# Optimization experiments

Hardware: AMD Instinct MI355X
Metric: run time of the kernel (lower is better)

Reference implementation:

```python
import jax, jax.numpy as jnp
import numpy as np

N = 100000
E = 1600000
D = 128


def setup_inputs() -> dict:
    key = jax.random.key(0)
    ks = jax.random.split(key, 16)
    inp = {
        "x": jax.random.normal(ks[0], (N, D), dtype=jnp.float32),
        "src": jax.random.randint(ks[1], (E,), 0, N, dtype=jnp.int32),
        "dst": jax.random.randint(ks[2], (E,), 0, N, dtype=jnp.int32),
    }
    scale = 1.0 / np.sqrt(D)
    for i in range(4):
        inp[f"ws{i}"] = jax.random.normal(ks[3 + 3 * i], (D, D), dtype=jnp.float32) * scale
        inp[f"wn{i}"] = jax.random.normal(ks[4 + 3 * i], (D, D), dtype=jnp.float32) * scale
        inp[f"b{i}"] = jnp.zeros((D,), dtype=jnp.float32)
    return inp


def _sage_layer(h, src, dst, w_self, w_neigh, b):
    # gather source-node features along edges, mean-reduce by destination
    msg = jnp.take(h, src, axis=0)                                   # [E, D]
    agg = jax.ops.segment_sum(msg, dst, num_segments=N)              # [N, D]
    deg = jax.ops.segment_sum(jnp.ones_like(dst, dtype=h.dtype), dst, num_segments=N)
    mean = agg / jnp.maximum(deg, 1.0)[:, None]                      # zero-degree -> 0
    return h @ w_self + mean @ w_neigh + b


def reference(x, src, dst, ws0, wn0, b0, ws1, wn1, b1, ws2, wn2, b2, ws3, wn3, b3):
    h = jax.nn.relu(_sage_layer(x, src, dst, ws0, wn0, b0))
    h = jax.nn.relu(_sage_layer(h, src, dst, ws1, wn1, b1))
    h = jax.nn.relu(_sage_layer(h, src, dst, ws2, wn2, b2))
    h = _sage_layer(h, src, dst, ws3, wn3, b3)
    return h
```

## Files before the change

kernel.cpp:

```cpp
#include <hip/hip_runtime.h>

#define N_NODES 100000
#define N_EDGES 1600000
#define DIM 128

typedef __attribute__((ext_vector_type(8))) _Float16 f16x8;
typedef __attribute__((ext_vector_type(4))) float f32x4;

__device__ __forceinline__ void stage16(const _Float16* g, _Float16* l) {
  __builtin_amdgcn_global_load_lds(
      (const __attribute__((address_space(1))) void*)g,
      (__attribute__((address_space(3))) void*)l, 16, 0, 0);
}


__global__ void k_count(const int* __restrict__ dst, int* __restrict__ cnt) {
  int i = blockIdx.x * blockDim.x + threadIdx.x;
  if (i < N_EDGES) atomicAdd(&cnt[dst[i]], 1);
}

__global__ void k_scan_blk(const int* __restrict__ cnt, int* __restrict__ offs,
                           int* __restrict__ partials) {
  int tid = threadIdx.x;
  int gid = blockIdx.x * 1024 + tid;
  int v = (gid < N_NODES) ? cnt[gid] : 0;
  int lane = tid & 63, w = tid >> 6;
  int s = v;
#pragma unroll
  for (int d = 1; d < 64; d <<= 1) {
    int t = __shfl_up(s, d);
    if (lane >= d) s += t;
  }
  __shared__ int wsum[16];
  if (lane == 63) wsum[w] = s;
  __syncthreads();
  if (tid < 16) {
    int t2 = wsum[tid];
#pragma unroll
    for (int d = 1; d < 16; d <<= 1) {
      int u = __shfl_up(t2, d);
      if (tid >= d) t2 += u;
    }
    wsum[tid] = t2;
  }
  __syncthreads();
  if (w > 0) s += wsum[w - 1];
  if (gid < N_NODES) offs[gid + 1] = s;
  if (tid == 1023) partials[blockIdx.x] = s;
}

__global__ void k_scan_part(int* __restrict__ partials, int nb) {
  __shared__ int tmp[128];
  int tid = threadIdx.x;
  tmp[tid] = (tid < nb) ? partials[tid] : 0;
  __syncthreads();
  for (int d = 1; d < 128; d <<= 1) {
    int t = (tid >= d) ? tmp[tid - d] : 0;
    __syncthreads();
    tmp[tid] += t;
    __syncthreads();
  }
  if (tid < nb) partials[tid] = (tid > 0) ? tmp[tid - 1] : 0;
}

__global__ void k_scan_add(int* __restrict__ offs, const int* __restrict__ partials) {
  int i = blockIdx.x * blockDim.x + threadIdx.x;
  if (i == 0) offs[0] = 0;
  if (i < N_NODES) offs[i + 1] += partials[i >> 10];
}

__global__ void k_prep(const int* __restrict__ offs, const int* __restrict__ cnt,
                       int* __restrict__ cursor, float* __restrict__ deg_inv) {
  int i = blockIdx.x * blockDim.x + threadIdx.x;
  if (i < N_NODES) {
    cursor[i] = offs[i];
    deg_inv[i] = 1.0f / (float)max(cnt[i], 1);
  }
}

#define FILL_BPP 224
__global__ void k_fill8(const int* __restrict__ src, const int* __restrict__ dst,
                        int* __restrict__ cursor, int* __restrict__ esrc) {
  const int part = blockIdx.x & 7;
  const int bp = blockIdx.x >> 3;
  const int lo = part * (N_NODES / 8);
  const int hi = lo + (N_NODES / 8);
  for (int i = bp * 256 + threadIdx.x; i < N_EDGES; i += FILL_BPP * 256) {
    int d = dst[i];
    if (d >= lo && d < hi) {
      int p = atomicAdd(&cursor[d], 1);
      esrc[p] = src[i];
    }
  }
}


#define WP_MAT (4 * 8 * 64 * 8)
#define WP_LAYER (2 * WP_MAT)

#define NZ_BLOCKS ((N_NODES + 255) / 256)
#define NX_BLOCKS ((N_NODES * DIM / 4 + 255) / 256)
#define NW_BLOCKS 64

__global__ void k_preproc(int* __restrict__ cnt, const float* __restrict__ x,
                          _Float16* __restrict__ x1, _Float16* __restrict__ x2,
                          const float* __restrict__ ws0, const float* __restrict__ wn0,
                          const float* __restrict__ ws1, const float* __restrict__ wn1,
                          const float* __restrict__ ws2, const float* __restrict__ wn2,
                          const float* __restrict__ ws3, const float* __restrict__ wn3,
                          _Float16* __restrict__ wp) {
  const int bid = blockIdx.x;
  if (bid < NZ_BLOCKS) {
    int i = bid * 256 + threadIdx.x;
    if (i < N_NODES) cnt[i] = 0;
  } else if (bid < NZ_BLOCKS + NX_BLOCKS) {
    int i = (bid - NZ_BLOCKS) * 256 + threadIdx.x;
    if (i < (N_NODES * DIM) / 4) {
      float4 v = reinterpret_cast<const float4*>(x)[i];
      union { _Float16 h[4]; uint2 u; } a, b;
      float vv[4] = {v.x, v.y, v.z, v.w};
#pragma unroll
      for (int j = 0; j < 4; ++j) {
        _Float16 h1 = (_Float16)vv[j];
        a.h[j] = h1;
        b.h[j] = (_Float16)(vv[j] - (float)h1);
      }
      reinterpret_cast<uint2*>(x1)[i] = a.u;
      reinterpret_cast<uint2*>(x2)[i] = b.u;
    }
  } else {
    int tid = (bid - NZ_BLOCKS - NX_BLOCKS) * 256 + threadIdx.x;
    int l = tid & 63;
    int f = (tid >> 6) & 7;
    int t = (tid >> 9) & 3;
    int m = (tid >> 11) & 1;
    int layer = tid >> 12;
    const float* srcs[8] = {ws0, wn0, ws1, wn1, ws2, wn2, ws3, wn3};
    const float* src = srcs[layer * 2 + m];
    _Float16* dstp =
        wp + (size_t)layer * WP_LAYER + ((((m * 4 + t) * 8 + f) * 64 + l) * 8);
    int k0 = t * 32 + (l >> 4) * 8;
    int col = f * 16 + (l & 15);
#pragma unroll
    for (int j = 0; j < 8; ++j) dstp[j] = (_Float16)src[(k0 + j) * DIM + col];
  }
}


__device__ __forceinline__ float f16lo(unsigned w) {
  union { unsigned u; _Float16 h[2]; } c;
  c.u = w;
  return (float)c.h[0];
}
__device__ __forceinline__ float f16hi(unsigned w) {
  union { unsigned u; _Float16 h[2]; } c;
  c.u = w;
  return (float)c.h[1];
}

__global__ void k_agg_f16(const _Float16* __restrict__ h1, const int* __restrict__ offs,
                          const int* __restrict__ esrc, const float* __restrict__ deg_inv,
                          _Float16* __restrict__ m1) {
  int wid = (blockIdx.x * blockDim.x + threadIdx.x) >> 6;
  int lane = threadIdx.x & 63;
  if (wid >= N_NODES) return;
  const unsigned* H = reinterpret_cast<const unsigned*>(h1);
  int beg = offs[wid], end = offs[wid + 1];
  float xs[8] = {0.f, 0.f, 0.f, 0.f, 0.f, 0.f, 0.f, 0.f};
  float ys[8] = {0.f, 0.f, 0.f, 0.f, 0.f, 0.f, 0.f, 0.f};
  int e = beg;
  for (; e + 7 < end; e += 8) {
    int s[8];
#pragma unroll
    for (int j = 0; j < 8; ++j) s[j] = esrc[e + j];
    unsigned w[8];
#pragma unroll
    for (int j = 0; j < 8; ++j) w[j] = H[(size_t)s[j] * 64 + lane];
#pragma unroll
    for (int j = 0; j < 8; ++j) {
      xs[j] += f16lo(w[j]);
      ys[j] += f16hi(w[j]);
    }
  }
  for (; e + 1 < end; e += 2) {
    unsigned w0 = H[(size_t)esrc[e] * 64 + lane];
    unsigned w1 = H[(size_t)esrc[e + 1] * 64 + lane];
    xs[0] += f16lo(w0); ys[0] += f16hi(w0);
    xs[1] += f16lo(w1); ys[1] += f16hi(w1);
  }
  if (e < end) {
    unsigned w0 = H[(size_t)esrc[e] * 64 + lane];
    xs[2] += f16lo(w0); ys[2] += f16hi(w0);
  }
  float di = deg_inv[wid];
  float rx = ((xs[0] + xs[1]) + (xs[2] + xs[3])) + ((xs[4] + xs[5]) + (xs[6] + xs[7]));
  float ry = ((ys[0] + ys[1]) + (ys[2] + ys[3])) + ((ys[4] + ys[5]) + (ys[6] + ys[7]));
  rx *= di;
  ry *= di;
  union { unsigned u; _Float16 h[2]; } o;
  o.h[0] = (_Float16)rx;
  o.h[1] = (_Float16)ry;
  reinterpret_cast<unsigned*>(m1)[(size_t)wid * 64 + lane] = o.u;
}


template <int RELU, int LAST>
__global__ __launch_bounds__(256, 3) void k_gemm_f16(
    const _Float16* __restrict__ hp1, const _Float16* __restrict__ hp2,
    const _Float16* __restrict__ mp1, const _Float16* __restrict__ wp,
    const float* __restrict__ bias, float* __restrict__ outf,
    _Float16* __restrict__ o1, _Float16* __restrict__ o2) {
  __shared__ _Float16 sA[3][64 * 128];

  const int tid = threadIdx.x;
  const int lane = tid & 63;
  const int wv = tid >> 6;
  const int wr = wv >> 1;
  const int wc = wv & 1;
  const int row0 = blockIdx.x * 64;
  const int lr = lane & 15;
  const int lg = lane >> 4;

  const _Float16* planes[3] = {hp1, hp2, mp1};

#pragma unroll
  for (int p = 0; p < 3; ++p)
#pragma unroll
    for (int i = 0; i < 4; ++i) {
      int s = i * 256 + tid;
      int row = s >> 4;
      int chunk = (s & 15) ^ (row & 7);
      const _Float16* g = planes[p] + (size_t)(row0 + row) * DIM + chunk * 8;
      _Float16* l = &sA[p][(size_t)(i * 256 + (tid & ~63)) * 8];
      stage16(g, l);
    }
  __syncthreads();

  f32x4 acc[2][4];
#pragma unroll
  for (int i = 0; i < 2; ++i)
#pragma unroll
    for (int j = 0; j < 4; ++j) acc[i][j] = (f32x4){0.f, 0.f, 0.f, 0.f};

  const _Float16* WS1 = wp;
  const _Float16* WN1 = wp + WP_MAT;

#pragma unroll
  for (int t = 0; t < 4; ++t) {
    f16x8 a1[2], a2[2], am[2];
#pragma unroll
    for (int ri = 0; ri < 2; ++ri) {
      int row_l = wr * 32 + ri * 16 + lr;
      int boff = (row_l << 8) + ((t * 64 + lg * 16) ^ ((row_l & 7) << 4));
      a1[ri] = *reinterpret_cast<const f16x8*>(
          reinterpret_cast<const char*>(&sA[0][0]) + boff);
      a2[ri] = *reinterpret_cast<const f16x8*>(
          reinterpret_cast<const char*>(&sA[1][0]) + boff);
      am[ri] = *reinterpret_cast<const f16x8*>(
          reinterpret_cast<const char*>(&sA[2][0]) + boff);
    }
#pragma unroll
    for (int fc = 0; fc < 4; ++fc) {
      int f = wc * 4 + fc;
      size_t boff = (size_t)((t * 8 + f) * 64 + lane) * 8;
      f16x8 bs1 = *reinterpret_cast<const f16x8*>(WS1 + boff);
      f16x8 bn1 = *reinterpret_cast<const f16x8*>(WN1 + boff);
#pragma unroll
      for (int ri = 0; ri < 2; ++ri) {
        acc[ri][fc] =
            __builtin_amdgcn_mfma_f32_16x16x32_f16(a1[ri], bs1, acc[ri][fc], 0, 0, 0);
        acc[ri][fc] =
            __builtin_amdgcn_mfma_f32_16x16x32_f16(a2[ri], bs1, acc[ri][fc], 0, 0, 0);
        acc[ri][fc] =
            __builtin_amdgcn_mfma_f32_16x16x32_f16(am[ri], bn1, acc[ri][fc], 0, 0, 0);
      }
    }
  }

  float bv[4];
#pragma unroll
  for (int fc = 0; fc < 4; ++fc) bv[fc] = bias[wc * 64 + fc * 16 + lr];
#pragma unroll
  for (int ri = 0; ri < 2; ++ri)
#pragma unroll
    for (int fc = 0; fc < 4; ++fc)
#pragma unroll
      for (int r = 0; r < 4; ++r) {
        int row = row0 + wr * 32 + ri * 16 + lg * 4 + r;
        if (row < N_NODES) {
          float v = acc[ri][fc][r] + bv[fc];
          if (RELU) v = fmaxf(v, 0.f);
          size_t idx = (size_t)row * DIM + wc * 64 + fc * 16 + lr;
          if (LAST) {
            outf[idx] = v;
          } else {
            _Float16 hi = (_Float16)v;
            o1[idx] = hi;
            o2[idx] = (_Float16)(v - (float)hi);
          }
        }
      }
}


extern "C" void kernel_launch(void* const* d_in, const int* in_sizes, int n_in,
                              void* d_out, int out_size, void* d_ws, size_t ws_size,
                              hipStream_t stream) {
  const float* x = (const float*)d_in[0];
  const int* src = (const int*)d_in[1];
  const int* dst = (const int*)d_in[2];
  const float* Ws[4];
  const float* Wn[4];
  const float* Bi[4];
  for (int i = 0; i < 4; ++i) {
    Ws[i] = (const float*)d_in[3 + 3 * i];
    Wn[i] = (const float*)d_in[4 + 3 * i];
    Bi[i] = (const float*)d_in[5 + 3 * i];
  }
  float* out = (float*)d_out;

  char* p = (char*)d_ws;
  auto take = [&](size_t bytes) {
    void* r = (void*)p;
    p += (bytes + 255) & ~(size_t)255;
    return r;
  };
  int* cnt = (int*)take((size_t)N_NODES * 4);
  int* offs = (int*)take((size_t)(N_NODES + 1) * 4);
  int* cursor = (int*)take((size_t)N_NODES * 4);
  int* partials = (int*)take(128 * 4);
  float* deg_inv = (float*)take((size_t)N_NODES * 4);
  int* esrc = (int*)take((size_t)N_EDGES * 4);
  _Float16* hA1 = (_Float16*)take((size_t)N_NODES * DIM * 2);
  _Float16* hA2 = (_Float16*)take((size_t)N_NODES * DIM * 2);
  _Float16* hB1 = (_Float16*)take((size_t)N_NODES * DIM * 2);
  _Float16* hB2 = (_Float16*)take((size_t)N_NODES * DIM * 2);
  _Float16* m1 = (_Float16*)take((size_t)N_NODES * DIM * 2);
  _Float16* wpk = (_Float16*)take((size_t)4 * WP_LAYER * 2);
  (void)take((size_t)64 * 1024);

  const int NB = (N_NODES + 1023) / 1024;

  k_preproc<<<NZ_BLOCKS + NX_BLOCKS + NW_BLOCKS, 256, 0, stream>>>(
      cnt, x, hA1, hA2, Ws[0], Wn[0], Ws[1], Wn[1], Ws[2], Wn[2], Ws[3], Wn[3], wpk);

  k_count<<<(N_EDGES + 255) / 256, 256, 0, stream>>>(dst, cnt);
  k_scan_blk<<<NB, 1024, 0, stream>>>(cnt, offs, partials);
  k_scan_part<<<1, 128, 0, stream>>>(partials, NB);
  k_scan_add<<<(N_NODES + 255) / 256, 256, 0, stream>>>(offs, partials);
  k_prep<<<(N_NODES + 255) / 256, 256, 0, stream>>>(offs, cnt, cursor, deg_inv);
  k_fill8<<<8 * FILL_BPP, 256, 0, stream>>>(src, dst, cursor, esrc);

  const int AGG_BLOCKS = (N_NODES + 3) / 4;
  const int GEMM_BLOCKS = (N_NODES + 63) / 64;

  _Float16 *h1 = hA1, *h2 = hA2, *n1 = hB1, *n2 = hB2;
  for (int l = 0; l < 4; ++l) {
    k_agg_f16<<<AGG_BLOCKS, 256, 0, stream>>>(h1, offs, esrc, deg_inv, m1);
    const _Float16* wl = wpk + (size_t)l * WP_LAYER;
    if (l < 3) {
      k_gemm_f16<1, 0><<<GEMM_BLOCKS, 256, 0, stream>>>(h1, h2, m1, wl, Bi[l], nullptr,
                                                        n1, n2);
      _Float16* t1 = h1; h1 = n1; n1 = t1;
      _Float16* t2 = h2; h2 = n2; n2 = t2;
    } else {
      k_gemm_f16<0, 1><<<GEMM_BLOCKS, 256, 0, stream>>>(h1, h2, m1, wl, Bi[l], out,
                                                        nullptr, nullptr);
    }
  }
}
```

Before: 552.4 us.

## Slice hi-half features into 16-column planes for cache-local aggregation

Stores the fp16 high part of node features in a column-sliced layout with 8 planes of 16 features per node. The aggregation kernel now runs one block group per slice, so each wave gathers 32-byte pieces from a 3.2 MB plane that can stay cache-resident, and combines partial sums across 8 edge groups with shuffles. The GEMM loader and epilogue are updated to read and write the sliced layout. In exchange it launches 8x more aggregation blocks, re-reads the edge index list once per slice, and the GEMM's hi-part stores become more scattered.

```diff
diff --git a/kernel.cpp b/kernel.cpp
--- a/kernel.cpp
+++ b/kernel.cpp
@@ -103,7 +103,7 @@
 #define NW_BLOCKS 64
 
 __global__ void k_preproc(int* __restrict__ cnt, const float* __restrict__ x,
-                          _Float16* __restrict__ x1, _Float16* __restrict__ x2,
+                          _Float16* __restrict__ x1t, _Float16* __restrict__ x2,
                           const float* __restrict__ ws0, const float* __restrict__ wn0,
                           const float* __restrict__ ws1, const float* __restrict__ wn1,
                           const float* __restrict__ ws2, const float* __restrict__ wn2,
@@ -125,7 +125,11 @@
         a.h[j] = h1;
         b.h[j] = (_Float16)(vv[j] - (float)h1);
       }
-      reinterpret_cast<uint2*>(x1)[i] = a.u;
+      int flat = i * 4;
+      int n = flat >> 7;
+      int d = flat & 127;
+      _Float16* dsta = x1t + ((size_t)(d >> 4) * N_NODES + n) * 16 + (d & 15);
+      *reinterpret_cast<uint2*>(dsta) = a.u;
       reinterpret_cast<uint2*>(x2)[i] = b.u;
     }
   } else {
@@ -158,58 +162,59 @@
   return (float)c.h[1];
 }
 
-__global__ void k_agg_f16(const _Float16* __restrict__ h1, const int* __restrict__ offs,
-                          const int* __restrict__ esrc, const float* __restrict__ deg_inv,
-                          _Float16* __restrict__ m1) {
-  int wid = (blockIdx.x * blockDim.x + threadIdx.x) >> 6;
-  int lane = threadIdx.x & 63;
-  if (wid >= N_NODES) return;
-  const unsigned* H = reinterpret_cast<const unsigned*>(h1);
-  int beg = offs[wid], end = offs[wid + 1];
-  float xs[8] = {0.f, 0.f, 0.f, 0.f, 0.f, 0.f, 0.f, 0.f};
-  float ys[8] = {0.f, 0.f, 0.f, 0.f, 0.f, 0.f, 0.f, 0.f};
-  int e = beg;
-  for (; e + 7 < end; e += 8) {
-    int s[8];
-#pragma unroll
-    for (int j = 0; j < 8; ++j) s[j] = esrc[e + j];
-    unsigned w[8];
-#pragma unroll
-    for (int j = 0; j < 8; ++j) w[j] = H[(size_t)s[j] * 64 + lane];
-#pragma unroll
-    for (int j = 0; j < 8; ++j) {
-      xs[j] += f16lo(w[j]);
-      ys[j] += f16hi(w[j]);
-    }
-  }
-  for (; e + 1 < end; e += 2) {
-    unsigned w0 = H[(size_t)esrc[e] * 64 + lane];
-    unsigned w1 = H[(size_t)esrc[e + 1] * 64 + lane];
-    xs[0] += f16lo(w0); ys[0] += f16hi(w0);
-    xs[1] += f16lo(w1); ys[1] += f16hi(w1);
-  }
-  if (e < end) {
-    unsigned w0 = H[(size_t)esrc[e] * 64 + lane];
-    xs[2] += f16lo(w0); ys[2] += f16hi(w0);
-  }
-  float di = deg_inv[wid];
-  float rx = ((xs[0] + xs[1]) + (xs[2] + xs[3])) + ((xs[4] + xs[5]) + (xs[6] + xs[7]));
-  float ry = ((ys[0] + ys[1]) + (ys[2] + ys[3])) + ((ys[4] + ys[5]) + (ys[6] + ys[7]));
-  rx *= di;
-  ry *= di;
-  union { unsigned u; _Float16 h[2]; } o;
-  o.h[0] = (_Float16)rx;
-  o.h[1] = (_Float16)ry;
-  reinterpret_cast<unsigned*>(m1)[(size_t)wid * 64 + lane] = o.u;
+__global__ __launch_bounds__(256) void k_agg_t(
+    const _Float16* __restrict__ h1t, const int* __restrict__ offs,
+    const int* __restrict__ esrc, const float* __restrict__ deg_inv,
+    _Float16* __restrict__ m1) {
+  const int slice = blockIdx.x & 7;
+  const int node = (blockIdx.x >> 3) * 4 + (threadIdx.x >> 6);
+  if (node >= N_NODES) return;
+  const int lane = threadIdx.x & 63;
+  const int g = lane >> 3;
+  const int d = lane & 7;
+  const unsigned* T =
+      reinterpret_cast<const unsigned*>(h1t) + (size_t)slice * N_NODES * 8;
+  int beg = offs[node], end = offs[node + 1];
+  float ax = 0.f, ay = 0.f, bx = 0.f, by = 0.f;
+  for (int e = beg; e < end; e += 16) {
+    int e0 = e + g;
+    int e1 = e + 8 + g;
+    if (e0 < end) {
+      int s0 = __builtin_nontemporal_load(esrc + e0);
+      unsigned w0 = T[(size_t)s0 * 8 + d];
+      ax += f16lo(w0);
+      ay += f16hi(w0);
+    }
+    if (e1 < end) {
+      int s1 = __builtin_nontemporal_load(esrc + e1);
+      unsigned w1 = T[(size_t)s1 * 8 + d];
+      bx += f16lo(w1);
+      by += f16hi(w1);
+    }
+  }
+  ax += bx;
+  ay += by;
+#pragma unroll
+  for (int m = 8; m < 64; m <<= 1) {
+    ax += __shfl_xor(ax, m);
+    ay += __shfl_xor(ay, m);
+  }
+  if (lane < 8) {
+    float di = deg_inv[node];
+    union { unsigned u; _Float16 h[2]; } o;
+    o.h[0] = (_Float16)(ax * di);
+    o.h[1] = (_Float16)(ay * di);
+    reinterpret_cast<unsigned*>(m1)[(size_t)node * 64 + slice * 8 + d] = o.u;
+  }
 }
 
 
 template <int RELU, int LAST>
 __global__ __launch_bounds__(256, 3) void k_gemm_f16(
-    const _Float16* __restrict__ hp1, const _Float16* __restrict__ hp2,
+    const _Float16* __restrict__ h1t, const _Float16* __restrict__ hp2,
     const _Float16* __restrict__ mp1, const _Float16* __restrict__ wp,
     const float* __restrict__ bias, float* __restrict__ outf,
-    _Float16* __restrict__ o1, _Float16* __restrict__ o2) {
+    _Float16* __restrict__ o1t, _Float16* __restrict__ o2) {
   __shared__ _Float16 sA[3][64 * 128];
 
   const int tid = threadIdx.x;
@@ -221,18 +226,25 @@
   const int lr = lane & 15;
   const int lg = lane >> 4;
 
-  const _Float16* planes[3] = {hp1, hp2, mp1};
-
-#pragma unroll
-  for (int p = 0; p < 3; ++p)
+#pragma unroll
+  for (int i = 0; i < 4; ++i) {
+    int s = i * 256 + tid;
+    int row = s >> 4;
+    int chunk = (s & 15) ^ (row & 7);
+    const _Float16* g0 =
+        h1t + ((size_t)(chunk >> 1) * N_NODES + (row0 + row)) * 16 + (chunk & 1) * 8;
+    stage16(g0, &sA[0][(size_t)(i * 256 + (tid & ~63)) * 8]);
+  }
+  const _Float16* planes12[2] = {hp2, mp1};
+#pragma unroll
+  for (int p = 0; p < 2; ++p)
 #pragma unroll
     for (int i = 0; i < 4; ++i) {
       int s = i * 256 + tid;
       int row = s >> 4;
       int chunk = (s & 15) ^ (row & 7);
-      const _Float16* g = planes[p] + (size_t)(row0 + row) * DIM + chunk * 8;
-      _Float16* l = &sA[p][(size_t)(i * 256 + (tid & ~63)) * 8];
-      stage16(g, l);
+      const _Float16* g = planes12[p] + (size_t)(row0 + row) * DIM + chunk * 8;
+      stage16(g, &sA[1 + p][(size_t)(i * 256 + (tid & ~63)) * 8]);
     }
   __syncthreads();
 
@@ -290,13 +302,12 @@
         if (row < N_NODES) {
           float v = acc[ri][fc][r] + bv[fc];
           if (RELU) v = fmaxf(v, 0.f);
-          size_t idx = (size_t)row * DIM + wc * 64 + fc * 16 + lr;
           if (LAST) {
-            outf[idx] = v;
+            outf[(size_t)row * DIM + wc * 64 + fc * 16 + lr] = v;
           } else {
             _Float16 hi = (_Float16)v;
-            o1[idx] = hi;
-            o2[idx] = (_Float16)(v - (float)hi);
+            o1t[((size_t)(wc * 4 + fc) * N_NODES + row) * 16 + lr] = hi;
+            o2[(size_t)row * DIM + wc * 64 + fc * 16 + lr] = (_Float16)(v - (float)hi);
           }
         }
       }
@@ -331,10 +342,10 @@
   int* partials = (int*)take(128 * 4);
   float* deg_inv = (float*)take((size_t)N_NODES * 4);
   int* esrc = (int*)take((size_t)N_EDGES * 4);
-  _Float16* hA1 = (_Float16*)take((size_t)N_NODES * DIM * 2);
-  _Float16* hA2 = (_Float16*)take((size_t)N_NODES * DIM * 2);
-  _Float16* hB1 = (_Float16*)take((size_t)N_NODES * DIM * 2);
-  _Float16* hB2 = (_Float16*)take((size_t)N_NODES * DIM * 2);
+  _Float16* h1tA = (_Float16*)take((size_t)8 * N_NODES * 16 * 2);
+  _Float16* h1tB = (_Float16*)take((size_t)8 * N_NODES * 16 * 2);
+  _Float16* h2A = (_Float16*)take((size_t)N_NODES * DIM * 2);
+  _Float16* h2B = (_Float16*)take((size_t)N_NODES * DIM * 2);
   _Float16* m1 = (_Float16*)take((size_t)N_NODES * DIM * 2);
   _Float16* wpk = (_Float16*)take((size_t)4 * WP_LAYER * 2);
   (void)take((size_t)64 * 1024);
@@ -342,7 +353,7 @@
   const int NB = (N_NODES + 1023) / 1024;
 
   k_preproc<<<NZ_BLOCKS + NX_BLOCKS + NW_BLOCKS, 256, 0, stream>>>(
-      cnt, x, hA1, hA2, Ws[0], Wn[0], Ws[1], Wn[1], Ws[2], Wn[2], Ws[3], Wn[3], wpk);
+      cnt, x, h1tA, h2A, Ws[0], Wn[0], Ws[1], Wn[1], Ws[2], Wn[2], Ws[3], Wn[3], wpk);
 
   k_count<<<(N_EDGES + 255) / 256, 256, 0, stream>>>(dst, cnt);
   k_scan_blk<<<NB, 1024, 0, stream>>>(cnt, offs, partials);
@@ -351,12 +362,12 @@
   k_prep<<<(N_NODES + 255) / 256, 256, 0, stream>>>(offs, cnt, cursor, deg_inv);
   k_fill8<<<8 * FILL_BPP, 256, 0, stream>>>(src, dst, cursor, esrc);
 
-  const int AGG_BLOCKS = (N_NODES + 3) / 4;
+  const int AGG_BLOCKS = (N_NODES / 4) * 8;
   const int GEMM_BLOCKS = (N_NODES + 63) / 64;
 
-  _Float16 *h1 = hA1, *h2 = hA2, *n1 = hB1, *n2 = hB2;
+  _Float16 *h1 = h1tA, *h2 = h2A, *n1 = h1tB, *n2 = h2B;
   for (int l = 0; l < 4; ++l) {
-    k_agg_f16<<<AGG_BLOCKS, 256, 0, stream>>>(h1, offs, esrc, deg_inv, m1);
+    k_agg_t<<<AGG_BLOCKS, 256, 0, stream>>>(h1, offs, esrc, deg_inv, m1);
     const _Float16* wl = wpk + (size_t)l * WP_LAYER;
     if (l < 3) {
       k_gemm_f16<1, 0><<<GEMM_BLOCKS, 256, 0, stream>>>(h1, h2, m1, wl, Bi[l], nullptr,
```

After: 1.468 ms. 2.66x slower.
